# Performance work log

Hardware: AMD Instinct MI355X
Metric: run time of the kernel (lower is better)

The kernel has to match this reference:

```python
import jax, jax.numpy as jnp
import numpy as np

B, S, D_MODEL, H = 4, 1024, 1024, 16
HD = D_MODEL // H  # head_dim = 64


def setup_inputs() -> dict:
    key = jax.random.key(0)
    ks = jax.random.split(key, 12)
    sd = 1.0 / np.sqrt(D_MODEL)
    return {
        "x": jax.random.normal(ks[0], (B, S, D_MODEL), dtype=jnp.float32),
        "Wq": jax.random.normal(ks[1], (D_MODEL, D_MODEL), dtype=jnp.float32) * sd,
        "bq": jnp.zeros((D_MODEL,), dtype=jnp.float32),
        "Wk": jax.random.normal(ks[2], (D_MODEL, D_MODEL), dtype=jnp.float32) * sd,
        "bk": jnp.zeros((D_MODEL,), dtype=jnp.float32),
        "Wv": jax.random.normal(ks[3], (D_MODEL, D_MODEL), dtype=jnp.float32) * sd,
        "bv": jnp.zeros((D_MODEL,), dtype=jnp.float32),
        "W1": jax.random.normal(ks[4], (2 * D_MODEL, D_MODEL), dtype=jnp.float32) * sd,
        "b1": jnp.zeros((2 * D_MODEL,), dtype=jnp.float32),
        "W2": jax.random.normal(ks[5], (D_MODEL, 2 * D_MODEL), dtype=jnp.float32) * (1.0 / np.sqrt(2 * D_MODEL)),
        "b2": jnp.zeros((D_MODEL,), dtype=jnp.float32),
        "mask": jnp.ones((B, S, S), dtype=jnp.int32),
    }


def reference(x, Wq, bq, Wk, bk, Wv, bv, W1, b1, W2, b2, mask):
    # QKV projections (torch Linear: y = x @ W.T + b), split into heads -> [B,H,S,HD]
    def proj(W, b):
        return (x @ W.T + b).reshape(B, S, H, HD).transpose(0, 2, 1, 3)

    q = proj(Wq, bq)
    k = proj(Wk, bk)
    v = proj(Wv, bv)

    scores = jnp.einsum("bhqd,bhkd->bhqk", q, k) / jnp.sqrt(jnp.float32(HD))
    # mask [B,S,S] broadcast over heads (original does unsqueeze(1).repeat)
    scores = jnp.where(mask[:, None, :, :] == 0, jnp.float32(-1e8), scores)
    probs = jax.nn.softmax(scores, axis=-1)
    ctx = jnp.einsum("bhqk,bhkd->bhqd", probs, v)
    ctx = ctx.transpose(0, 2, 1, 3).reshape(B, S, D_MODEL)

    # out-projection MLP: Linear(d, 2d) -> ReLU -> Linear(2d, d)
    h = jax.nn.relu(ctx @ W1.T + b1)
    return h @ W2.T + b2
```

## Files before the change

kernel.cpp:

```cpp
#include <hip/hip_runtime.h>
#include <hip/hip_bf16.h>
#include <stdint.h>


#define B_ 4
#define S_ 1024
#define DM_ 1024
#define H_ 16
#define HD_ 64

typedef __attribute__((ext_vector_type(8))) short short8;
typedef __attribute__((ext_vector_type(4))) float f32x4;
typedef __attribute__((ext_vector_type(4))) unsigned short ushort4v;

#define GLB_AS(p) ((const __attribute__((address_space(1))) void*)(p))
#define LDS_AS(p) ((__attribute__((address_space(3))) void*)(p))

__device__ __forceinline__ void async_load16(const void* g, void* l) {
  __builtin_amdgcn_global_load_lds(GLB_AS(g), LDS_AS(l), 16, 0, 0);
}

__device__ __forceinline__ unsigned short f2bf(float x) {
  union { float f; unsigned int u; } v; v.f = x;
  unsigned int r = v.u + 0x7fffu + ((v.u >> 16) & 1u);
  return (unsigned short)(r >> 16);
}

#define QSCALE 0.18033688011112042f

struct PrepArgs {
  const float* src[6];
  unsigned short* dst[6];
  int n4[6];
  const int* mask;
  unsigned long long* bits;
  unsigned int* rowflag;
  const float* bq;
  const float* bk;
  const float* bv;
  float* cb;
};

__global__ void prep_kernel(PrepArgs a) {
  const int seg = blockIdx.y;
  if (seg < 6) {
    const int n4 = a.n4[seg];
    const f32x4* __restrict__ src = (const f32x4*)a.src[seg];
    ushort4v* __restrict__ dst = (ushort4v*)a.dst[seg];
    for (int i = blockIdx.x * blockDim.x + threadIdx.x; i < n4;
         i += gridDim.x * blockDim.x) {
      f32x4 v = src[i];
      ushort4v o;
      o[0] = f2bf(v[0]); o[1] = f2bf(v[1]); o[2] = f2bf(v[2]); o[3] = f2bf(v[3]);
      dst[i] = o;
    }
  } else if (seg == 6) {
    const int wave = threadIdx.x >> 6;
    const int lane = threadIdx.x & 63;
#pragma unroll
    for (int rr = 0; rr < 4; ++rr) {
      const int row = blockIdx.x * 16 + wave * 4 + rr;
      const int* mr = a.mask + (size_t)row * S_;
      unsigned long long allf = ~0ull;
#pragma unroll
      for (int g = 0; g < 16; ++g) {
        int mv = mr[g * 64 + lane];
        unsigned long long bal = __ballot(mv != 0);
        if (lane == g) a.bits[(size_t)row * 16 + g] = bal;
        allf &= bal;
      }
      if (lane == 0) a.rowflag[row] = (allf == ~0ull) ? 1u : 0u;
    }
  } else {
    const int i = blockIdx.x * 256 + threadIdx.x;
    if (i < 3072) {
      const float* src = (i < 1024) ? a.bq : (i < 2048) ? a.bk : a.bv;
      a.cb[i] = src[i & 1023];
    }
  }
}

enum { EPI_QKV = 0, EPI_RELU_BF16 = 2, EPI_F32 = 3, EPI_PARTIAL = 4 };

template <int EPI>
__global__ __launch_bounds__(256, 3) void gemm_bt(
    const unsigned short* __restrict__ A, const unsigned short* __restrict__ Bt,
    const float* __restrict__ bias, void* __restrict__ Cp,
    unsigned short* __restrict__ Vt, int M, int N, int K, int Kld) {
  __shared__ __align__(16) unsigned short smem[128 * 136];
  unsigned short* sA = smem;
  unsigned short* sB = smem + 128 * 64;

  const int tid = threadIdx.x;
  const int lane = tid & 63;
  const int wave = tid >> 6;
  const int quad = lane >> 4;
  const int l15 = lane & 15;
  const int swzb = l15 & 7;
  const int m0 = blockIdx.y * 128;
  const int n0 = blockIdx.x * 128;
  const int wm = (wave >> 1) * 64;
  const int wn = (wave & 1) * 64;
  const int kz = blockIdx.z * K;

  f32x4 acc[4][4];
#pragma unroll
  for (int i = 0; i < 4; ++i)
#pragma unroll
    for (int j = 0; j < 4; ++j) acc[i][j] = (f32x4){0.f, 0.f, 0.f, 0.f};

  const int srow = tid >> 3;
  const int scol = ((tid & 7) ^ (srow & 7)) * 8;
  const unsigned short* gA = A + (size_t)(m0 + srow) * Kld + kz + scol;
  const unsigned short* gB = Bt + (size_t)(n0 + srow) * Kld + kz + scol;
  unsigned short* lA = sA + tid * 8;
  unsigned short* lB = sB + tid * 8;

  for (int k0 = 0; k0 < K; k0 += 64) {
    __syncthreads();
#pragma unroll
    for (int st = 0; st < 4; ++st) {
      async_load16(gA + (size_t)(st * 32) * Kld + k0, lA + st * 2048);
      async_load16(gB + (size_t)(st * 32) * Kld + k0, lB + st * 2048);
    }
    __syncthreads();

#pragma unroll
    for (int ks = 0; ks < 2; ++ks) {
      short8 af[4], bfr[4];
#pragma unroll
      for (int t = 0; t < 4; ++t) {
        const int cg = ((ks * 4 + quad) ^ swzb) * 8;
        af[t] = *(const short8*)(sA + (wm + t * 16 + l15) * 64 + cg);
        bfr[t] = *(const short8*)(sB + (wn + t * 16 + l15) * 64 + cg);
      }
#pragma unroll
      for (int mt = 0; mt < 4; ++mt)
#pragma unroll
        for (int nt = 0; nt < 4; ++nt)
          acc[mt][nt] = __builtin_amdgcn_mfma_f32_16x16x32_bf16(
              af[mt], bfr[nt], acc[mt][nt], 0, 0, 0);
    }
  }

  if (EPI == EPI_QKV && n0 >= 2048) {
    __syncthreads();
#pragma unroll
    for (int nt = 0; nt < 4; ++nt) {
      const int col = n0 + wn + nt * 16 + l15;
      const float bv = bias[col];
#pragma unroll
      for (int mt = 0; mt < 4; ++mt)
#pragma unroll
        for (int r = 0; r < 4; ++r)
          smem[(wn + nt * 16 + l15) * 136 + wm + mt * 16 + quad * 4 + r] =
              f2bf(acc[mt][nt][r] + bv);
    }
    __syncthreads();
    const int vc0 = n0 - 2048;
    const int bb = m0 >> 10;
    const int s0 = m0 & 1023;
#pragma unroll
    for (int i = 0; i < 8; ++i) {
      const int c = i * 16 + (tid >> 4);
      const int tc = tid & 15;
      const short8 val = *(const short8*)(smem + c * 136 + tc * 8);
      const int ch = vc0 + c;
      const int hh = ch >> 6, dd = ch & 63;
      *(short8*)(Vt + ((size_t)(bb * 16 + hh) * HD_ + dd) * S_ + s0 + tc * 8) =
          val;
    }
    return;
  }

#pragma unroll
  for (int nt = 0; nt < 4; ++nt) {
    const int col = n0 + wn + nt * 16 + l15;
    const float bv = (EPI == EPI_PARTIAL) ? 0.f : bias[col];
    const float scl = (EPI == EPI_QKV && col < 1024) ? QSCALE : 1.0f;
#pragma unroll
    for (int mt = 0; mt < 4; ++mt) {
#pragma unroll
      for (int r = 0; r < 4; ++r) {
        const int row = m0 + wm + mt * 16 + quad * 4 + r;
        float v = acc[mt][nt][r] + bv;
        if (EPI == EPI_F32) {
          ((float*)Cp)[(size_t)row * N + col] = v;
        } else if (EPI == EPI_PARTIAL) {
          ((float*)Cp)[(size_t)blockIdx.z * M * N + (size_t)row * N + col] = v;
        } else if (EPI == EPI_RELU_BF16) {
          ((unsigned short*)Cp)[(size_t)row * N + col] = f2bf(fmaxf(v, 0.f));
        } else {
          ((unsigned short*)Cp)[(size_t)row * N + col] = f2bf(v * scl);
        }
      }
    }
  }
}

__global__ __launch_bounds__(256, 2) void flash_attn(
    const unsigned short* __restrict__ Cqkv, const unsigned short* __restrict__ Vt,
    const unsigned long long* __restrict__ mbits,
    const unsigned int* __restrict__ mrowflag,
    unsigned short* __restrict__ ctx) {
  __shared__ unsigned short sK[128 * 64];
  __shared__ unsigned short sV[64 * 128];
  __shared__ unsigned short spb[4][32 * 136];

  const int tid = threadIdx.x;
  const int wave = tid >> 6;
  const int lane = tid & 63;
  const int quad = lane >> 4;
  const int l15 = lane & 15;
  const int bh = blockIdx.x;
  const int b = bh >> 4;
  const int h = bh & 15;
  const int qbase = blockIdx.y * 128 + wave * 32;

  const unsigned short* Qb = Cqkv + (size_t)(b * S_) * 3072 + h * HD_;
  const unsigned short* Kb = Cqkv + (size_t)(b * S_) * 3072 + DM_ + h * HD_;
  const unsigned short* Vb = Vt + (size_t)bh * HD_ * S_;
  unsigned short* pbuf = spb[wave];

  bool mask_all_ones;
  {
    unsigned int f = mrowflag[b * S_ + qbase + (lane & 31)];
    mask_all_ones = (__ballot(f != 0) == ~0ull);
  }

  short8 qf[2][2];
#pragma unroll
  for (int u = 0; u < 2; ++u)
#pragma unroll
    for (int ks = 0; ks < 2; ++ks)
      qf[u][ks] = *(const short8*)(Qb + (size_t)(qbase + u * 16 + l15) * 3072 +
                                   ks * 32 + quad * 8);

  f32x4 o[2][4];
#pragma unroll
  for (int u = 0; u < 2; ++u)
#pragma unroll
    for (int i = 0; i < 4; ++i) o[u][i] = (f32x4){0.f, 0.f, 0.f, 0.f};
  float lsum[2][4] = {{0.f, 0.f, 0.f, 0.f}, {0.f, 0.f, 0.f, 0.f}};

  for (int kt = 0; kt < S_ / 128; ++kt) {
    const int kbase = kt * 128;

    __syncthreads();
#pragma unroll
    for (int st = 0; st < 4; ++st) {
      const int j = st * 256 + tid;
      const int r = j >> 3, c = j & 7;
      async_load16(Kb + (size_t)(kbase + r) * 3072 + ((c ^ (r & 7)) * 8),
                   sK + j * 8);
    }
#pragma unroll
    for (int st = 0; st < 4; ++st) {
      const int j = st * 256 + tid;
      const int d = j >> 4, c = j & 15;
      async_load16(Vb + (size_t)d * S_ + kbase + ((c ^ (d & 15)) * 8),
                   sV + j * 8);
    }
    __syncthreads();

    f32x4 s[2][8];
#pragma unroll
    for (int u = 0; u < 2; ++u)
#pragma unroll
      for (int i = 0; i < 8; ++i) s[u][i] = (f32x4){0.f, 0.f, 0.f, 0.f};
#pragma unroll
    for (int ks = 0; ks < 2; ++ks) {
      const int cg = ks * 4 + quad;
#pragma unroll
      for (int nt = 0; nt < 8; ++nt) {
        const int row = nt * 16 + l15;
        const short8 kf =
            *(const short8*)(sK + row * 64 + ((cg ^ (row & 7)) * 8));
        s[0][nt] = __builtin_amdgcn_mfma_f32_16x16x32_bf16(qf[0][ks], kf,
                                                           s[0][nt], 0, 0, 0);
        s[1][nt] = __builtin_amdgcn_mfma_f32_16x16x32_bf16(qf[1][ks], kf,
                                                           s[1][nt], 0, 0, 0);
      }
    }

    if (!mask_all_ones) {
#pragma unroll
      for (int u = 0; u < 2; ++u)
#pragma unroll
        for (int r = 0; r < 4; ++r) {
          const int q = qbase + u * 16 + quad * 4 + r;
          const unsigned long long* wp =
              mbits + ((size_t)(b * S_ + q)) * 16 + kt * 2;
          const unsigned long long w0 = wp[0], w1 = wp[1];
#pragma unroll
          for (int nt = 0; nt < 8; ++nt) {
            const unsigned long long w = (nt < 4) ? w0 : w1;
            const int bit = (nt * 16 + l15) & 63;
            if (!((w >> bit) & 1)) s[u][nt][r] = -1.0e8f;
          }
        }
    }

#pragma unroll
    for (int u = 0; u < 2; ++u)
#pragma unroll
      for (int nt = 0; nt < 8; ++nt)
#pragma unroll
        for (int r = 0; r < 4; ++r) {
          const float p = __builtin_amdgcn_exp2f(s[u][nt][r]);
          lsum[u][r] += p;
          pbuf[(u * 16 + quad * 4 + r) * 136 + nt * 16 + l15] = f2bf(p);
        }

#pragma unroll
    for (int ks2 = 0; ks2 < 4; ++ks2) {
      const short8 pf0 =
          *(const short8*)(pbuf + l15 * 136 + ks2 * 32 + quad * 8);
      const short8 pf1 =
          *(const short8*)(pbuf + (16 + l15) * 136 + ks2 * 32 + quad * 8);
      const int cg = ks2 * 4 + quad;
#pragma unroll
      for (int nt = 0; nt < 4; ++nt) {
        const int d = nt * 16 + l15;
        const short8 vf =
            *(const short8*)(sV + d * 128 + ((cg ^ (d & 15)) * 8));
        o[0][nt] = __builtin_amdgcn_mfma_f32_16x16x32_bf16(pf0, vf, o[0][nt], 0, 0, 0);
        o[1][nt] = __builtin_amdgcn_mfma_f32_16x16x32_bf16(pf1, vf, o[1][nt], 0, 0, 0);
      }
    }
  }

#pragma unroll
  for (int u = 0; u < 2; ++u)
#pragma unroll
    for (int r = 0; r < 4; ++r) {
      float lr = lsum[u][r];
      lr += __shfl_xor(lr, 1);
      lr += __shfl_xor(lr, 2);
      lr += __shfl_xor(lr, 4);
      lr += __shfl_xor(lr, 8);
      const float inv = 1.0f / lr;
#pragma unroll
      for (int nt = 0; nt < 4; ++nt)
        pbuf[(u * 16 + quad * 4 + r) * 68 + nt * 16 + l15] =
            f2bf(o[u][nt][r] * inv);
    }
#pragma unroll
  for (int i = 0; i < 4; ++i) {
    const int j = i * 64 + lane;
    const int r = j >> 3, c = j & 7;
    const short8 val = *(const short8*)(pbuf + r * 68 + c * 8);
    *(short8*)(ctx + ((size_t)b * S_ + qbase + r) * DM_ + h * HD_ + c * 8) = val;
  }
}

__global__ void reduce_ffn2_kernel(const float* __restrict__ part,
                                   const float* __restrict__ b2,
                                   float* __restrict__ out) {
  const int i = blockIdx.x * 256 + threadIdx.x;
  const f32x4 a = ((const f32x4*)part)[i];
  const f32x4 b = ((const f32x4*)part)[i + (B_ * S_ * DM_ / 4)];
  const f32x4 bb = ((const f32x4*)b2)[i & 255];
  ((f32x4*)out)[i] = a + b + bb;
}

extern "C" void kernel_launch(void* const* d_in, const int* in_sizes, int n_in,
                              void* d_out, int out_size, void* d_ws,
                              size_t ws_size, hipStream_t stream) {
  const float* x = (const float*)d_in[0];
  const float* Wq = (const float*)d_in[1];
  const float* bq = (const float*)d_in[2];
  const float* Wk = (const float*)d_in[3];
  const float* bk = (const float*)d_in[4];
  const float* Wv = (const float*)d_in[5];
  const float* bv = (const float*)d_in[6];
  const float* W1 = (const float*)d_in[7];
  const float* b1 = (const float*)d_in[8];
  const float* W2 = (const float*)d_in[9];
  const float* b2 = (const float*)d_in[10];
  const int* mask = (const int*)d_in[11];
  float* out = (float*)d_out;

  char* ws = (char*)d_ws;
  unsigned short* xb   = (unsigned short*)(ws + 0);
  unsigned short* wqkv = (unsigned short*)(ws + 8388608);
  unsigned short* w1b  = (unsigned short*)(ws + 14680064);
  unsigned short* w2b  = (unsigned short*)(ws + 18874368);
  unsigned short* Cqkv = (unsigned short*)(ws + 23068672);
  unsigned short* ctxb = (unsigned short*)(ws + 48234496);
  unsigned short* hb   = (unsigned short*)(ws + 56623104);
  unsigned short* Vt   = (unsigned short*)(ws + 56623104);
  unsigned long long* mbits = (unsigned long long*)(ws + 73400320);
  unsigned int* mrowflag    = (unsigned int*)(ws + 73924608);
  float* cb                 = (float*)(ws + 73940992);
  float* part = (float*)(ws + 23068672);

  PrepArgs pa;
  pa.src[0] = x;  pa.dst[0] = xb;               pa.n4[0] = (B_ * S_ * DM_) / 4;
  pa.src[1] = Wq; pa.dst[1] = wqkv;             pa.n4[1] = (DM_ * DM_) / 4;
  pa.src[2] = Wk; pa.dst[2] = wqkv + DM_ * DM_; pa.n4[2] = (DM_ * DM_) / 4;
  pa.src[3] = Wv; pa.dst[3] = wqkv + 2 * DM_ * DM_; pa.n4[3] = (DM_ * DM_) / 4;
  pa.src[4] = W1; pa.dst[4] = w1b;              pa.n4[4] = (2 * DM_ * DM_) / 4;
  pa.src[5] = W2; pa.dst[5] = w2b;              pa.n4[5] = (2 * DM_ * DM_) / 4;
  pa.mask = mask; pa.bits = mbits; pa.rowflag = mrowflag;
  pa.bq = bq; pa.bk = bk; pa.bv = bv; pa.cb = cb;
  prep_kernel<<<dim3(256, 8), 256, 0, stream>>>(pa);

  const int M = B_ * S_;
  gemm_bt<EPI_QKV><<<dim3(3 * DM_ / 128, M / 128), 256, 0, stream>>>(
      xb, wqkv, cb, Cqkv, Vt, M, 3 * DM_, DM_, DM_);

  flash_attn<<<dim3(B_ * H_, S_ / 128), 256, 0, stream>>>(
      Cqkv, Vt, mbits, mrowflag, ctxb);

  gemm_bt<EPI_RELU_BF16><<<dim3((2 * DM_) / 128, M / 128), 256, 0, stream>>>(
      ctxb, w1b, b1, hb, nullptr, M, 2 * DM_, DM_, DM_);

  gemm_bt<EPI_PARTIAL><<<dim3(DM_ / 128, M / 128, 2), 256, 0, stream>>>(
      hb, w2b, b2, part, nullptr, M, DM_, DM_, 2 * DM_);
  reduce_ffn2_kernel<<<dim3(M * DM_ / 4 / 256), 256, 0, stream>>>(part, b2, out);
}
```

Measured before the change: 256.0 us.

## Halve flash-attn P staging buffer, raise occupancy, vectorize mask bit-packing

The flash attention kernel now stages one 16-row P tile at a time per wave and runs the PV MFMAs for it before writing the next, which halves the per-wave LDS staging buffer. That allows launch bounds of three blocks per CU instead of two. The mask prep now reads int4 vectors, packs 16 bits per lane and combines them with shuffles, one row per wave, and the prep grid grows to 1024 blocks so each block covers fewer rows. The trade-off is that the V fragments are reread from LDS for each 16-row half, and the tighter register budget may cause spills.

```diff
diff --git a/kernel.cpp b/kernel.cpp
--- a/kernel.cpp
+++ b/kernel.cpp
@@ -57,20 +57,23 @@
   } else if (seg == 6) {
     const int wave = threadIdx.x >> 6;
     const int lane = threadIdx.x & 63;
-#pragma unroll
-    for (int rr = 0; rr < 4; ++rr) {
-      const int row = blockIdx.x * 16 + wave * 4 + rr;
-      const int* mr = a.mask + (size_t)row * S_;
-      unsigned long long allf = ~0ull;
-#pragma unroll
-      for (int g = 0; g < 16; ++g) {
-        int mv = mr[g * 64 + lane];
-        unsigned long long bal = __ballot(mv != 0);
-        if (lane == g) a.bits[(size_t)row * 16 + g] = bal;
-        allf &= bal;
-      }
-      if (lane == 0) a.rowflag[row] = (allf == ~0ull) ? 1u : 0u;
-    }
+    const int row = blockIdx.x * 4 + wave;
+    const int4* mr = (const int4*)(a.mask + (size_t)row * S_) + lane * 4;
+    unsigned int chunk = 0;
+#pragma unroll
+    for (int t = 0; t < 4; ++t) {
+      const int4 v = mr[t];
+      chunk |= (v.x != 0 ? 1u : 0u) << (4 * t + 0);
+      chunk |= (v.y != 0 ? 1u : 0u) << (4 * t + 1);
+      chunk |= (v.z != 0 ? 1u : 0u) << (4 * t + 2);
+      chunk |= (v.w != 0 ? 1u : 0u) << (4 * t + 3);
+    }
+    unsigned long long v64 = (unsigned long long)chunk << (16 * (lane & 3));
+    v64 |= __shfl_xor(v64, 1);
+    v64 |= __shfl_xor(v64, 2);
+    if ((lane & 3) == 0) a.bits[(size_t)row * 16 + (lane >> 2)] = v64;
+    const bool all1 = (__ballot(chunk == 0xffffu) == ~0ull);
+    if (lane == 0) a.rowflag[row] = all1 ? 1u : 0u;
   } else {
     const int i = blockIdx.x * 256 + threadIdx.x;
     if (i < 3072) {
@@ -198,14 +201,14 @@
   }
 }
 
-__global__ __launch_bounds__(256, 2) void flash_attn(
+__global__ __launch_bounds__(256, 3) void flash_attn(
     const unsigned short* __restrict__ Cqkv, const unsigned short* __restrict__ Vt,
     const unsigned long long* __restrict__ mbits,
     const unsigned int* __restrict__ mrowflag,
     unsigned short* __restrict__ ctx) {
   __shared__ unsigned short sK[128 * 64];
   __shared__ unsigned short sV[64 * 128];
-  __shared__ unsigned short spb[4][32 * 136];
+  __shared__ unsigned short spb[4][16 * 136];
 
   const int tid = threadIdx.x;
   const int wave = tid >> 6;
@@ -302,30 +305,28 @@
     }
 
 #pragma unroll
-    for (int u = 0; u < 2; ++u)
+    for (int u = 0; u < 2; ++u) {
 #pragma unroll
       for (int nt = 0; nt < 8; ++nt)
 #pragma unroll
         for (int r = 0; r < 4; ++r) {
           const float p = __builtin_amdgcn_exp2f(s[u][nt][r]);
           lsum[u][r] += p;
-          pbuf[(u * 16 + quad * 4 + r) * 136 + nt * 16 + l15] = f2bf(p);
+          pbuf[(quad * 4 + r) * 136 + nt * 16 + l15] = f2bf(p);
         }
-
-#pragma unroll
-    for (int ks2 = 0; ks2 < 4; ++ks2) {
-      const short8 pf0 =
-          *(const short8*)(pbuf + l15 * 136 + ks2 * 32 + quad * 8);
-      const short8 pf1 =
-          *(const short8*)(pbuf + (16 + l15) * 136 + ks2 * 32 + quad * 8);
-      const int cg = ks2 * 4 + quad;
-#pragma unroll
-      for (int nt = 0; nt < 4; ++nt) {
-        const int d = nt * 16 + l15;
-        const short8 vf =
-            *(const short8*)(sV + d * 128 + ((cg ^ (d & 15)) * 8));
-        o[0][nt] = __builtin_amdgcn_mfma_f32_16x16x32_bf16(pf0, vf, o[0][nt], 0, 0, 0);
-        o[1][nt] = __builtin_amdgcn_mfma_f32_16x16x32_bf16(pf1, vf, o[1][nt], 0, 0, 0);
+#pragma unroll
+      for (int ks2 = 0; ks2 < 4; ++ks2) {
+        const short8 pf =
+            *(const short8*)(pbuf + l15 * 136 + ks2 * 32 + quad * 8);
+        const int cg = ks2 * 4 + quad;
+#pragma unroll
+        for (int nt = 0; nt < 4; ++nt) {
+          const int d = nt * 16 + l15;
+          const short8 vf =
+              *(const short8*)(sV + d * 128 + ((cg ^ (d & 15)) * 8));
+          o[u][nt] =
+              __builtin_amdgcn_mfma_f32_16x16x32_bf16(pf, vf, o[u][nt], 0, 0, 0);
+        }
       }
     }
   }
@@ -404,7 +405,7 @@
   pa.src[5] = W2; pa.dst[5] = w2b;              pa.n4[5] = (2 * DM_ * DM_) / 4;
   pa.mask = mask; pa.bits = mbits; pa.rowflag = mrowflag;
   pa.bq = bq; pa.bk = bk; pa.bv = bv; pa.cb = cb;
-  prep_kernel<<<dim3(256, 8), 256, 0, stream>>>(pa);
+  prep_kernel<<<dim3(1024, 8), 256, 0, stream>>>(pa);
 
   const int M = B_ * S_;
   gemm_bt<EPI_QKV><<<dim3(3 * DM_ / 128, M / 128), 256, 0, stream>>>(
```

Result: faster. 247.9 us (-3.1%).
